# Kernel optimization log

Measured on AMD Instinct MI355X. Metric: run time of the kernel, lower is better.

## Reference

```python
import jax, jax.numpy as jnp
import numpy as np
from jax import lax

EPS = 1e-5

def _dsconv(x, dw, pw, g, b, m, v, relu):
    # x: [B,C,H,W]; dw: [C,1,3,3] depthwise; pw: [C,C,1,1] pointwise; eval-mode BN
    C = x.shape[1]
    y = lax.conv_general_dilated(x, dw, (1, 1), 'SAME', feature_group_count=C)
    y = lax.conv_general_dilated(y, pw, (1, 1), 'SAME')
    scale = (g * lax.rsqrt(v + EPS))[None, :, None, None]
    y = y * scale + (b - m * g * lax.rsqrt(v + EPS))[None, :, None, None]
    return jnp.maximum(y, 0.0) if relu else y

def _attention(x, wq, bq, wk, bk, wv, bv, gamma):
    b, c, h, w = x.shape
    n = h * w
    xf = x.reshape(b, c, n)                      # [B,C,N]
    q = jnp.einsum('oc,bcn->bon', wq, xf) + bq[None, :, None]   # [B,C/8,N]
    k = jnp.einsum('oc,bcn->bon', wk, xf) + bk[None, :, None]   # [B,C/8,N]
    v = jnp.einsum('oc,bcn->bon', wv, xf) + bv[None, :, None]   # [B,C,N]
    logits = jnp.einsum('bdm,bdn->bmn', q, k)    # q^T k, [B,N,N]
    attn = jax.nn.softmax(logits, axis=2)
    out = jnp.einsum('bcn,bmn->bcm', v, attn).reshape(b, c, h, w)
    return gamma[0] * out + x

def setup_inputs() -> dict:
    key = jax.random.key(0)
    ks = jax.random.split(key, 20)
    B, C, H, W = 64, 256, 32, 32
    C8 = C // 8
    rn = lambda k, s, sc: (jax.random.normal(k, s, dtype=jnp.float32) * sc)
    return {
        'x': rn(ks[0], (B, C, H, W), 1.0),
        'dw1': rn(ks[1], (C, 1, 3, 3), 0.2),
        'pw1': rn(ks[2], (C, C, 1, 1), 0.06),
        'bn1_g': jax.random.uniform(ks[3], (C,), jnp.float32, 0.5, 1.5),
        'bn1_b': rn(ks[4], (C,), 0.1),
        'bn1_m': rn(ks[5], (C,), 0.1),
        'bn1_v': jax.random.uniform(ks[6], (C,), jnp.float32, 0.5, 1.5),
        'dw2': rn(ks[7], (C, 1, 3, 3), 0.2),
        'pw2': rn(ks[8], (C, C, 1, 1), 0.06),
        'bn2_g': jax.random.uniform(ks[9], (C,), jnp.float32, 0.5, 1.5),
        'bn2_b': rn(ks[10], (C,), 0.1),
        'bn2_m': rn(ks[11], (C,), 0.1),
        'bn2_v': jax.random.uniform(ks[12], (C,), jnp.float32, 0.5, 1.5),
        'wq': rn(ks[13], (C8, C), 0.06),
        'bq': rn(ks[14], (C8,), 0.02),
        'wk': rn(ks[15], (C8, C), 0.06),
        'bk': rn(ks[16], (C8,), 0.02),
        'wv': rn(ks[17], (C, C), 0.06),
        'bv': rn(ks[18], (C,), 0.02),
        'gamma': rn(ks[19], (1,), 0.5),
    }

def reference(x, dw1, pw1, bn1_g, bn1_b, bn1_m, bn1_v,
              dw2, pw2, bn2_g, bn2_b, bn2_m, bn2_v,
              wq, bq, wk, bk, wv, bv, gamma):
    out = _dsconv(x, dw1, pw1, bn1_g, bn1_b, bn1_m, bn1_v, relu=True)
    out = _dsconv(out, dw2, pw2, bn2_g, bn2_b, bn2_m, bn2_v, relu=False)
    out = _attention(out + x, wq, bq, wk, bk, wv, bv, gamma)
    return jnp.maximum(out, 0.0)
```

## Files before the change

kernel.cpp:

```cpp
#include <hip/hip_runtime.h>
#include <cstdint>
#include <cstddef>

#define B_ 64
#define C_ 256
#define N_ 1024
#define LOG2E 1.4426950408889634f

typedef short v8s __attribute__((ext_vector_type(8)));
typedef float v4f __attribute__((ext_vector_type(4)));
typedef unsigned int u32;
typedef unsigned short u16;

__device__ __forceinline__ float bf2f(u16 u) {
  return __uint_as_float(((u32)u) << 16);
}
__device__ __forceinline__ u16 f2bf(float f) {
  u32 x = __float_as_uint(f);
  x += 0x7fffu + ((x >> 16) & 1u);
  return (u16)(x >> 16);
}
__device__ __forceinline__ u32 pack2(float a, float b) {
  return (u32)f2bf(a) | ((u32)f2bf(b) << 16);
}

typedef __attribute__((address_space(3))) unsigned int lds_as_t;
typedef __attribute__((address_space(1))) const unsigned int glb_as_t;
__device__ __forceinline__ void ld_lds16(const u16* g, u16* l) {
  __builtin_amdgcn_global_load_lds((glb_as_t*)g, (lds_as_t*)l, 16, 0, 0);
}

__global__ __launch_bounds__(256) void prep(
    const float* __restrict__ g1, const float* __restrict__ b1,
    const float* __restrict__ m1, const float* __restrict__ v1,
    const float* __restrict__ g2, const float* __restrict__ b2,
    const float* __restrict__ m2, const float* __restrict__ v2,
    const float* __restrict__ wq, const float* __restrict__ bq,
    const float* __restrict__ wk, const float* __restrict__ bk,
    const float* __restrict__ wv, const float* __restrict__ bv,
    const float* __restrict__ pw1, const float* __restrict__ pw2,
    const float* __restrict__ dw1, const float* __restrict__ dw2,
    float* __restrict__ scale1, float* __restrict__ shift1,
    float* __restrict__ scale2, float* __restrict__ shift2,
    float* __restrict__ dwT1, float* __restrict__ dwT2,
    u16* __restrict__ pw1b, u16* __restrict__ pw2b, u16* __restrict__ wcatb,
    float* __restrict__ bcat) {
  const int gt = blockIdx.x * 256 + threadIdx.x;
  if (gt < 256) {
    float s1 = g1[gt] * rsqrtf(v1[gt] + 1e-5f);
    scale1[gt] = s1;
    shift1[gt] = b1[gt] - m1[gt] * s1;
    float s2 = g2[gt] * rsqrtf(v2[gt] + 1e-5f);
    scale2[gt] = s2;
    shift2[gt] = b2[gt] - m2[gt] * s2;
  }
  if (gt < 320)
    bcat[gt] = (gt < 32) ? bq[gt] * LOG2E
                         : (gt < 64) ? bk[gt - 32] : bv[gt - 64];
  if (gt < 2304) {
    dwT1[(gt % 9) * 256 + gt / 9] = dw1[gt];
    dwT2[(gt % 9) * 256 + gt / 9] = dw2[gt];
  }
  for (int e = gt; e < 65536; e += 16384) {
    pw1b[e] = f2bf(pw1[e]);
    pw2b[e] = f2bf(pw2[e]);
  }
  for (int e = gt; e < 81920; e += 16384) {
    const int o = e >> 8;
    float w = (o < 32) ? wq[e] * LOG2E
                       : (o < 64) ? wk[e - 8192] : wv[e - 16384];
    wcatb[e] = f2bf(w);
  }
}

__global__ __launch_bounds__(256) void transpose_x(const float* __restrict__ x,
                                                   u16* __restrict__ xt) {
  __shared__ float t[64][65];
  const int b = blockIdx.z, c0 = blockIdx.y * 64, n0 = blockIdx.x * 64;
  const float* xp = x + ((size_t)b * C_ + c0) * N_ + n0;
  const int tn = threadIdx.x & 63, tc = threadIdx.x >> 6;
#pragma unroll
  for (int i = 0; i < 16; ++i)
    t[tc + 4 * i][tn] = xp[(size_t)(tc + 4 * i) * N_ + tn];
  __syncthreads();
  u16* op = xt + ((size_t)b * N_ + n0) * C_ + c0;
  const int oc = threadIdx.x & 63, on = threadIdx.x >> 6;
#pragma unroll
  for (int i = 0; i < 16; ++i)
    op[(size_t)(on + 4 * i) * C_ + oc] = f2bf(t[oc][on + 4 * i]);
}

__global__ __launch_bounds__(256) void dw_nhwc(const u16* __restrict__ src,
                                               const float* __restrict__ wT,
                                               u16* __restrict__ dst) {
  __shared__ float wl[9][256];
  const int b = blockIdx.y;
  for (int e = threadIdx.x; e < 2304; e += 256) wl[e >> 8][e & 255] = wT[e];
  __syncthreads();
  const int pl = threadIdx.x >> 5, c0 = (threadIdx.x & 31) * 8;
  const int p = blockIdx.x * 8 + pl;
  const int h = p >> 5, wx = p & 31;
  const u16* sp = src + (size_t)b * N_ * C_;
  float acc[8] = {0.f, 0.f, 0.f, 0.f, 0.f, 0.f, 0.f, 0.f};
#pragma unroll
  for (int dh = -1; dh <= 1; ++dh) {
    const int hh = h + dh;
    if (hh < 0 || hh > 31) continue;
#pragma unroll
    for (int dx = -1; dx <= 1; ++dx) {
      const int ww = wx + dx;
      if (ww < 0 || ww > 31) continue;
      const int k = (dh + 1) * 3 + (dx + 1);
      const uint4 v = *(const uint4*)(sp + (size_t)(hh * 32 + ww) * C_ + c0);
      const u32 vv[4] = {v.x, v.y, v.z, v.w};
#pragma unroll
      for (int j = 0; j < 4; ++j) {
        acc[2 * j] += bf2f((u16)(vv[j] & 0xffffu)) * wl[k][c0 + 2 * j];
        acc[2 * j + 1] += bf2f((u16)(vv[j] >> 16)) * wl[k][c0 + 2 * j + 1];
      }
    }
  }
  uint4 o4;
  o4.x = pack2(acc[0], acc[1]);
  o4.y = pack2(acc[2], acc[3]);
  o4.z = pack2(acc[4], acc[5]);
  o4.w = pack2(acc[6], acc[7]);
  *(uint4*)(dst + ((size_t)b * N_ + p) * C_ + c0) = o4;
}

template <int EPI>
__global__ __launch_bounds__(256) void gemm(
    const u16* __restrict__ X, const u16* __restrict__ W,
    const float* __restrict__ scale, const float* __restrict__ shift,
    const u16* __restrict__ resid, u16* __restrict__ Y, u16* __restrict__ Y2) {
  __shared__ u16 smem[17408];
  u16(*Xs)[64] = (u16(*)[64])smem;
  u16(*Ws)[64] = (u16(*)[64])(smem + 8192);
  u16(*Ys)[136] = (u16(*)[136])smem;
  u16(*YsQ)[68] = (u16(*)[68])smem;

  const int tid = threadIdx.x;
  const int b = blockIdx.z;
  const int n0 = blockIdx.x * 128, o0 = blockIdx.y * 128;
  const int wid = tid >> 6, lane = tid & 63;
  const int wn = wid & 1, wo = wid >> 1;
  const int l15 = lane & 15, l4 = lane >> 4;
  const int lr = lane >> 3, lc = (lane & 7) * 8;

  v4f acc[4][4];
#pragma unroll
  for (int i = 0; i < 4; ++i)
#pragma unroll
    for (int j = 0; j < 4; ++j) acc[i][j] = v4f{0.f, 0.f, 0.f, 0.f};

  for (int k0 = 0; k0 < C_; k0 += 64) {
#pragma unroll
    for (int g = 0; g < 4; ++g) {
      const int base = wid * 32 + g * 8;
      ld_lds16(X + ((size_t)b * N_ + n0 + base + lr) * C_ + k0 + lc,
               &Xs[base][0]);
      int wr = o0 + base + lr;
      if (EPI == 2 && wr > 319) wr = 319;
      ld_lds16(W + (size_t)wr * C_ + k0 + lc, &Ws[base][0]);
    }
    __syncthreads();
#pragma unroll
    for (int ks = 0; ks < 2; ++ks) {
      v8s af[4], bf4[4];
#pragma unroll
      for (int f = 0; f < 4; ++f) {
        if constexpr (EPI != 2) {
          af[f] = *(const v8s*)&Ws[wo * 64 + f * 16 + l15][ks * 32 + l4 * 8];
          bf4[f] = *(const v8s*)&Xs[wn * 64 + f * 16 + l15][ks * 32 + l4 * 8];
        } else {
          af[f] = *(const v8s*)&Xs[wn * 64 + f * 16 + l15][ks * 32 + l4 * 8];
          bf4[f] = *(const v8s*)&Ws[wo * 64 + f * 16 + l15][ks * 32 + l4 * 8];
        }
      }
#pragma unroll
      for (int i = 0; i < 4; ++i)
#pragma unroll
        for (int j = 0; j < 4; ++j)
          acc[i][j] = __builtin_amdgcn_mfma_f32_16x16x32_bf16(
              af[i], bf4[j], acc[i][j], 0, 0, 0);
    }
    __syncthreads();
  }

  if constexpr (EPI != 2) {
#pragma unroll
    for (int i = 0; i < 4; ++i) {
      const int oL = wo * 64 + i * 16 + l4 * 4;
      const int o = o0 + oL;
      const float4 sc = *(const float4*)&scale[o];
      const float4 sh = *(const float4*)&shift[o];
#pragma unroll
      for (int j = 0; j < 4; ++j) {
        const int nL = wn * 64 + j * 16 + l15;
        float y0 = acc[i][j][0] * sc.x + sh.x;
        float y1 = acc[i][j][1] * sc.y + sh.y;
        float y2 = acc[i][j][2] * sc.z + sh.z;
        float y3 = acc[i][j][3] * sc.w + sh.w;
        if constexpr (EPI == 0) {
          y0 = fmaxf(y0, 0.f);
          y1 = fmaxf(y1, 0.f);
          y2 = fmaxf(y2, 0.f);
          y3 = fmaxf(y3, 0.f);
        } else {
          const uint2 rb =
              *(const uint2*)(resid + ((size_t)b * N_ + n0 + nL) * C_ + o);
          y0 += bf2f((u16)(rb.x & 0xffffu));
          y1 += bf2f((u16)(rb.x >> 16));
          y2 += bf2f((u16)(rb.y & 0xffffu));
          y3 += bf2f((u16)(rb.y >> 16));
        }
        uint2 st;
        st.x = pack2(y0, y1);
        st.y = pack2(y2, y3);
        *(uint2*)&Ys[nL][oL] = st;
      }
    }
    __syncthreads();
#pragma unroll
    for (int s = 0; s < 8; ++s) {
      const int nL = s * 16 + (tid >> 4);
      const int slot = tid & 15;
      const uint4 v = *(const uint4*)&Ys[nL][slot * 8];
      *(uint4*)&Y[((size_t)b * N_ + n0 + nL) * C_ + o0 + slot * 8] = v;
    }
  } else {
    float bj[4];
#pragma unroll
    for (int j = 0; j < 4; ++j) {
      int o = o0 + wo * 64 + j * 16 + l15;
      bj[j] = shift[o > 319 ? 319 : o];
    }
    if (o0 == 0 && wo == 0) {
#pragma unroll
      for (int i = 0; i < 4; ++i) {
        const int nL = wn * 64 + i * 16 + l4 * 4;
#pragma unroll
        for (int j = 0; j < 4; ++j) {
          const int oL = j * 16 + l15;
#pragma unroll
          for (int r = 0; r < 4; ++r) YsQ[nL + r][oL] = f2bf(acc[i][j][r] + bj[j]);
        }
      }
    } else {
#pragma unroll
      for (int i = 0; i < 4; ++i) {
        const int nL = wn * 64 + i * 16 + l4 * 4;
#pragma unroll
        for (int j = 0; j < 4; ++j) {
          const int oL = wo * 64 + j * 16 + l15;
          uint2 st;
          st.x = pack2(acc[i][j][0] + bj[j], acc[i][j][1] + bj[j]);
          st.y = pack2(acc[i][j][2] + bj[j], acc[i][j][3] + bj[j]);
          *(uint2*)&Ys[oL][nL] = st;
        }
      }
    }
    __syncthreads();
    if (o0 == 0) {
#pragma unroll
      for (int s = 0; s < 4; ++s) {
        const int e = s * 256 + tid;
        const int row = e >> 3, seg = e & 7;
        const uint4 v = *(const uint4*)&YsQ[row][seg * 8];
        *(uint4*)&Y[((size_t)b * N_ + n0 + row) * 64 + seg * 8] = v;
      }
#pragma unroll
      for (int s = 0; s < 4; ++s) {
        const int e = s * 256 + tid;
        const int oL = 64 + (e >> 4), slot = e & 15;
        const uint4 v = *(const uint4*)&Ys[oL][slot * 8];
        *(uint4*)&Y2[((size_t)b * C_ + oL - 64) * N_ + n0 + slot * 8] = v;
      }
    } else {
#pragma unroll
      for (int s = 0; s < 8; ++s) {
        const int oL = s * 16 + (tid >> 4);
        const int c = o0 + oL - 64;
        if (c < 256) {
          const int slot = tid & 15;
          const uint4 v = *(const uint4*)&Ys[oL][slot * 8];
          *(uint4*)&Y2[((size_t)b * C_ + c) * N_ + n0 + slot * 8] = v;
        }
      }
    }
  }
}

__global__ __launch_bounds__(256, 4) void flash(
    const u16* __restrict__ qk, const u16* __restrict__ vchw,
    const u16* __restrict__ abf, const float* __restrict__ gamma_p,
    float* __restrict__ out) {
  const int b = blockIdx.x;
  const int m0 = blockIdx.y * 64;
  const int tid = threadIdx.x, wid = tid >> 6, lane = tid & 63;
  const int l15 = lane & 15, l4 = lane >> 4;
  const int mw = m0 + wid * 16;

  __shared__ u16 Vs[2][256][32];
  __shared__ u16 Plds[4][16][36];

  const u16* qkb = qk + (size_t)b * N_ * 64;
  const u16* vb = vchw + (size_t)b * C_ * N_;
  const v8s qf = *(const v8s*)&qkb[(size_t)(mw + l15) * 64 + l4 * 8];

  const int s_row = lane >> 2;
  const int s_j = (lane & 3) ^ (s_row & 3);

#pragma unroll
  for (int g = 0; g < 4; ++g) {
    const int base = wid * 64 + g * 16;
    ld_lds16(vb + (size_t)(base + s_row) * N_ + s_j * 8, &Vs[0][base][0]);
  }

  float Mloc = -3e38f;
  {
    v8s kf[4];
#pragma unroll
    for (int f = 0; f < 4; ++f)
      kf[f] = *(const v8s*)&qkb[(size_t)(f * 16 + l15) * 64 + 32 + l4 * 8];
    for (int t = 0; t < 16; ++t) {
      v8s kn[4];
      if (t < 15) {
        const int n1 = (t + 1) * 64;
#pragma unroll
        for (int f = 0; f < 4; ++f)
          kn[f] =
              *(const v8s*)&qkb[(size_t)(n1 + f * 16 + l15) * 64 + 32 + l4 * 8];
      }
#pragma unroll
      for (int f = 0; f < 4; ++f) {
        const v4f lt = __builtin_amdgcn_mfma_f32_16x16x32_bf16(
            kf[f], qf, v4f{0.f, 0.f, 0.f, 0.f}, 0, 0, 0);
        Mloc = fmaxf(Mloc, fmaxf(fmaxf(lt[0], lt[1]), fmaxf(lt[2], lt[3])));
      }
      if (t < 15) {
#pragma unroll
        for (int f = 0; f < 4; ++f) kf[f] = kn[f];
      }
    }
  }
  Mloc = fmaxf(Mloc, __shfl_xor(Mloc, 16));
  Mloc = fmaxf(Mloc, __shfl_xor(Mloc, 32));
  const float M = Mloc;

  v4f acc[16];
#pragma unroll
  for (int i = 0; i < 16; ++i) acc[i] = v4f{0.f, 0.f, 0.f, 0.f};
  float S0 = 0.f, S1 = 0.f, S2 = 0.f, S3 = 0.f;
  v8s k2[2];
#pragma unroll
  for (int f = 0; f < 2; ++f)
    k2[f] = *(const v8s*)&qkb[(size_t)(f * 16 + l15) * 64 + 32 + l4 * 8];
  __syncthreads();

  for (int t = 0; t < 32; ++t) {
    const int cur = t & 1;
    const v4f lt0 = __builtin_amdgcn_mfma_f32_16x16x32_bf16(
        k2[0], qf, v4f{0.f, 0.f, 0.f, 0.f}, 0, 0, 0);
    const v4f lt1 = __builtin_amdgcn_mfma_f32_16x16x32_bf16(
        k2[1], qf, v4f{0.f, 0.f, 0.f, 0.f}, 0, 0, 0);
    if (t < 31) {
      const int n1 = (t + 1) * 32;
#pragma unroll
      for (int g = 0; g < 4; ++g) {
        const int base = wid * 64 + g * 16;
        ld_lds16(vb + (size_t)(base + s_row) * N_ + n1 + s_j * 8,
                 &Vs[cur ^ 1][base][0]);
      }
#pragma unroll
      for (int f = 0; f < 2; ++f)
        k2[f] =
            *(const v8s*)&qkb[(size_t)(n1 + f * 16 + l15) * 64 + 32 + l4 * 8];
    }
    {
      const float p0 = exp2f(lt0[0] - M);
      const float p1 = exp2f(lt0[1] - M);
      const float p2 = exp2f(lt0[2] - M);
      const float p3 = exp2f(lt0[3] - M);
      S0 += p0;
      S1 += p1;
      S2 += p2;
      S3 += p3;
      uint2 pw;
      pw.x = pack2(p0, p1);
      pw.y = pack2(p2, p3);
      *(uint2*)&Plds[wid][l15][l4 * 4] = pw;
    }
    {
      const float p0 = exp2f(lt1[0] - M);
      const float p1 = exp2f(lt1[1] - M);
      const float p2 = exp2f(lt1[2] - M);
      const float p3 = exp2f(lt1[3] - M);
      S0 += p0;
      S1 += p1;
      S2 += p2;
      S3 += p3;
      uint2 pw;
      pw.x = pack2(p0, p1);
      pw.y = pack2(p2, p3);
      *(uint2*)&Plds[wid][l15][16 + l4 * 4] = pw;
    }
    __builtin_amdgcn_sched_barrier(0);
    const v8s pa = *(const v8s*)&Plds[wid][l15][l4 * 8];
    __builtin_amdgcn_s_setprio(1);
#pragma unroll
    for (int cf = 0; cf < 16; ++cf) {
      const v8s vf = *(const v8s*)&Vs[cur][cf * 16 + l15][(l4 ^ (l15 & 3)) * 8];
      acc[cf] =
          __builtin_amdgcn_mfma_f32_16x16x32_bf16(pa, vf, acc[cf], 0, 0, 0);
    }
    __builtin_amdgcn_s_setprio(0);
    __syncthreads();
  }

  float S = (S0 + S1) + (S2 + S3);
  S += __shfl_xor(S, 16);
  S += __shfl_xor(S, 32);
  const float inv = 1.f / S;
  const float g = gamma_p[0];
  float invr[4];
#pragma unroll
  for (int r = 0; r < 4; ++r) invr[r] = __shfl(inv, l4 * 4 + r);
  const int mb = mw + l4 * 4;
#pragma unroll
  for (int cf = 0; cf < 16; ++cf) {
    const int c = cf * 16 + l15;
    float4 y;
    float* yp = (float*)&y;
#pragma unroll
    for (int r = 0; r < 4; ++r) {
      const float av = bf2f(abf[((size_t)b * N_ + mb + r) * C_ + c]);
      yp[r] = fmaxf(g * acc[cf][r] * invr[r] + av, 0.f);
    }
    *(float4*)&out[((size_t)b * C_ + c) * N_ + mb] = y;
  }
}

extern "C" void kernel_launch(void* const* d_in, const int* in_sizes, int n_in,
                              void* d_out, int out_size, void* d_ws,
                              size_t ws_size, hipStream_t stream) {
  const float* x = (const float*)d_in[0];
  const float* dw1 = (const float*)d_in[1];
  const float* pw1 = (const float*)d_in[2];
  const float* bn1g = (const float*)d_in[3];
  const float* bn1b = (const float*)d_in[4];
  const float* bn1m = (const float*)d_in[5];
  const float* bn1v = (const float*)d_in[6];
  const float* dw2 = (const float*)d_in[7];
  const float* pw2 = (const float*)d_in[8];
  const float* bn2g = (const float*)d_in[9];
  const float* bn2b = (const float*)d_in[10];
  const float* bn2m = (const float*)d_in[11];
  const float* bn2v = (const float*)d_in[12];
  const float* wq = (const float*)d_in[13];
  const float* bq = (const float*)d_in[14];
  const float* wk = (const float*)d_in[15];
  const float* bk = (const float*)d_in[16];
  const float* wv = (const float*)d_in[17];
  const float* bv = (const float*)d_in[18];
  const float* gamma = (const float*)d_in[19];
  float* out = (float*)d_out;

  char* ws = (char*)d_ws;
  size_t off = 0;
  auto alloc = [&](size_t bytes) {
    void* p = ws + off;
    off += (bytes + 255) & ~(size_t)255;
    return p;
  };
  const size_t NE = (size_t)B_ * N_ * C_;

  u16* bufA = (u16*)alloc(NE * 2);
  u16* bufB = (u16*)alloc(NE * 2);
  u16* bufC = (u16*)alloc(NE * 2);
  u16* abf = (u16*)alloc(NE * 2);
  float* scale1 = (float*)alloc(256 * 4);
  float* shift1 = (float*)alloc(256 * 4);
  float* scale2 = (float*)alloc(256 * 4);
  float* shift2 = (float*)alloc(256 * 4);
  float* dwT1 = (float*)alloc(2304 * 4);
  float* dwT2 = (float*)alloc(2304 * 4);
  u16* pw1b = (u16*)alloc(65536 * 2);
  u16* pw2b = (u16*)alloc(65536 * 2);
  u16* wcatb = (u16*)alloc(81920 * 2);
  float* bcat = (float*)alloc(384 * 4);

  u16* xt = bufA;
  u16* t1 = bufB;
  u16* y1 = bufC;
  u16* t2 = bufB;
  u16* qkbuf = bufC;
  u16* vchw = bufA;

  prep<<<64, 256, 0, stream>>>(bn1g, bn1b, bn1m, bn1v, bn2g, bn2b, bn2m, bn2v,
                               wq, bq, wk, bk, wv, bv, pw1, pw2, dw1, dw2,
                               scale1, shift1, scale2, shift2, dwT1, dwT2,
                               pw1b, pw2b, wcatb, bcat);
  transpose_x<<<dim3(16, 4, B_), 256, 0, stream>>>(x, xt);
  dw_nhwc<<<dim3(128, B_), 256, 0, stream>>>(xt, dwT1, t1);
  gemm<0><<<dim3(8, 2, B_), 256, 0, stream>>>(t1, pw1b, scale1, shift1,
                                              nullptr, y1, nullptr);
  dw_nhwc<<<dim3(128, B_), 256, 0, stream>>>(y1, dwT2, t2);
  gemm<1><<<dim3(8, 2, B_), 256, 0, stream>>>(t2, pw2b, scale2, shift2, xt,
                                              abf, nullptr);
  gemm<2><<<dim3(8, 3, B_), 256, 0, stream>>>(abf, wcatb, nullptr, bcat,
                                              nullptr, qkbuf, vchw);
  flash<<<dim3(64, 16), 256, 0, stream>>>(qkbuf, vchw, abf, gamma, out);
}
```

Baseline: 263.8 us.

## Restructure flash PV stage so each wave owns a channel quarter across all rows

```diff
diff --git a/kernel.cpp b/kernel.cpp
--- a/kernel.cpp
+++ b/kernel.cpp
@@ -300,22 +300,22 @@
   const int tid = threadIdx.x, wid = tid >> 6, lane = tid & 63;
   const int l15 = lane & 15, l4 = lane >> 4;
   const int mw = m0 + wid * 16;
-
-  __shared__ u16 Vs[2][256][32];
-  __shared__ u16 Plds[4][16][36];
+  const int cq = wid * 64;
+
+  __shared__ u16 Vs[256][40];
+  __shared__ u16 Pl[64][40];
+  __shared__ float Sl[64];
 
   const u16* qkb = qk + (size_t)b * N_ * 64;
   const u16* vb = vchw + (size_t)b * C_ * N_;
   const v8s qf = *(const v8s*)&qkb[(size_t)(mw + l15) * 64 + l4 * 8];
 
-  const int s_row = lane >> 2;
-  const int s_j = (lane & 3) ^ (s_row & 3);
-
-#pragma unroll
-  for (int g = 0; g < 4; ++g) {
-    const int base = wid * 64 + g * 16;
-    ld_lds16(vb + (size_t)(base + s_row) * N_ + s_j * 8, &Vs[0][base][0]);
-  }
+  const int vrow = tid >> 2, vslot = tid & 3;
+  uint4 vreg[4];
+#pragma unroll
+  for (int g = 0; g < 4; ++g)
+    vreg[g] =
+        *(const uint4*)(vb + (size_t)(vrow + 64 * g) * N_ + vslot * 8);
 
   float Mloc = -3e38f;
   {
@@ -348,9 +348,15 @@
   Mloc = fmaxf(Mloc, __shfl_xor(Mloc, 32));
   const float M = Mloc;
 
-  v4f acc[16];
-#pragma unroll
-  for (int i = 0; i < 16; ++i) acc[i] = v4f{0.f, 0.f, 0.f, 0.f};
+#pragma unroll
+  for (int g = 0; g < 4; ++g)
+    *(uint4*)&Vs[vrow + 64 * g][vslot * 8] = vreg[g];
+
+  v4f acc[4][4];
+#pragma unroll
+  for (int mf = 0; mf < 4; ++mf)
+#pragma unroll
+    for (int j = 0; j < 4; ++j) acc[mf][j] = v4f{0.f, 0.f, 0.f, 0.f};
   float S0 = 0.f, S1 = 0.f, S2 = 0.f, S3 = 0.f;
   v8s k2[2];
 #pragma unroll
@@ -359,19 +365,19 @@
   __syncthreads();
 
   for (int t = 0; t < 32; ++t) {
-    const int cur = t & 1;
+    if (t < 31) {
+      const int n1 = (t + 1) * 32;
+#pragma unroll
+      for (int g = 0; g < 4; ++g)
+        vreg[g] =
+            *(const uint4*)(vb + (size_t)(vrow + 64 * g) * N_ + n1 + vslot * 8);
+    }
     const v4f lt0 = __builtin_amdgcn_mfma_f32_16x16x32_bf16(
         k2[0], qf, v4f{0.f, 0.f, 0.f, 0.f}, 0, 0, 0);
     const v4f lt1 = __builtin_amdgcn_mfma_f32_16x16x32_bf16(
         k2[1], qf, v4f{0.f, 0.f, 0.f, 0.f}, 0, 0, 0);
     if (t < 31) {
       const int n1 = (t + 1) * 32;
-#pragma unroll
-      for (int g = 0; g < 4; ++g) {
-        const int base = wid * 64 + g * 16;
-        ld_lds16(vb + (size_t)(base + s_row) * N_ + n1 + s_j * 8,
-                 &Vs[cur ^ 1][base][0]);
-      }
 #pragma unroll
       for (int f = 0; f < 2; ++f)
         k2[f] =
@@ -389,7 +395,7 @@
       uint2 pw;
       pw.x = pack2(p0, p1);
       pw.y = pack2(p2, p3);
-      *(uint2*)&Plds[wid][l15][l4 * 4] = pw;
+      *(uint2*)&Pl[wid * 16 + l15][l4 * 4] = pw;
     }
     {
       const float p0 = exp2f(lt1[0] - M);
@@ -403,41 +409,60 @@
       uint2 pw;
       pw.x = pack2(p0, p1);
       pw.y = pack2(p2, p3);
-      *(uint2*)&Plds[wid][l15][16 + l4 * 4] = pw;
-    }
-    __builtin_amdgcn_sched_barrier(0);
-    const v8s pa = *(const v8s*)&Plds[wid][l15][l4 * 8];
+      *(uint2*)&Pl[wid * 16 + l15][16 + l4 * 4] = pw;
+    }
+    __syncthreads();
+    v8s pa[4];
+#pragma unroll
+    for (int mf = 0; mf < 4; ++mf)
+      pa[mf] = *(const v8s*)&Pl[mf * 16 + l15][l4 * 8];
     __builtin_amdgcn_s_setprio(1);
 #pragma unroll
-    for (int cf = 0; cf < 16; ++cf) {
-      const v8s vf = *(const v8s*)&Vs[cur][cf * 16 + l15][(l4 ^ (l15 & 3)) * 8];
-      acc[cf] =
-          __builtin_amdgcn_mfma_f32_16x16x32_bf16(pa, vf, acc[cf], 0, 0, 0);
+    for (int j = 0; j < 4; ++j) {
+      const v8s vf = *(const v8s*)&Vs[cq + j * 16 + l15][l4 * 8];
+#pragma unroll
+      for (int mf = 0; mf < 4; ++mf)
+        acc[mf][j] =
+            __builtin_amdgcn_mfma_f32_16x16x32_bf16(pa[mf], vf, acc[mf][j], 0,
+                                                    0, 0);
     }
     __builtin_amdgcn_s_setprio(0);
     __syncthreads();
+    if (t < 31) {
+#pragma unroll
+      for (int g = 0; g < 4; ++g)
+        *(uint4*)&Vs[vrow + 64 * g][vslot * 8] = vreg[g];
+    }
   }
 
   float S = (S0 + S1) + (S2 + S3);
   S += __shfl_xor(S, 16);
   S += __shfl_xor(S, 32);
-  const float inv = 1.f / S;
-  const float g = gamma_p[0];
-  float invr[4];
-#pragma unroll
-  for (int r = 0; r < 4; ++r) invr[r] = __shfl(inv, l4 * 4 + r);
-  const int mb = mw + l4 * 4;
-#pragma unroll
-  for (int cf = 0; cf < 16; ++cf) {
-    const int c = cf * 16 + l15;
-    float4 y;
-    float* yp = (float*)&y;
-#pragma unroll
-    for (int r = 0; r < 4; ++r) {
-      const float av = bf2f(abf[((size_t)b * N_ + mb + r) * C_ + c]);
-      yp[r] = fmaxf(g * acc[cf][r] * invr[r] + av, 0.f);
-    }
-    *(float4*)&out[((size_t)b * C_ + c) * N_ + mb] = y;
+  if (lane < 16) Sl[wid * 16 + lane] = 1.f / S;
+  __syncthreads();
+
+  const float gma = gamma_p[0];
+  float invv[4][4];
+#pragma unroll
+  for (int mf = 0; mf < 4; ++mf)
+#pragma unroll
+    for (int r = 0; r < 4; ++r) invv[mf][r] = Sl[mf * 16 + l4 * 4 + r];
+
+#pragma unroll
+  for (int mf = 0; mf < 4; ++mf) {
+    const int mb = m0 + mf * 16 + l4 * 4;
+#pragma unroll
+    for (int j = 0; j < 4; ++j) {
+      const int c = cq + j * 16 + l15;
+      float4 y;
+      float* yp = (float*)&y;
+#pragma unroll
+      for (int r = 0; r < 4; ++r) {
+        const float av = bf2f(abf[((size_t)b * N_ + mb + r) * C_ + c]);
+        yp[r] = fmaxf(gma * acc[mf][j][r] * invv[mf][r] + av, 0.f);
+      }
+      *(float4*)&out[((size_t)b * C_ + c) * N_ + mb] = y;
+    }
   }
 }
 
```

Measured after the change: 385.8 us. +46.3%, slower.
